# Optimization experiments

Measured on AMD Instinct MI355X. Metric: run time of the kernel, lower is better.

## Reference

```python
import jax, jax.numpy as jnp
import numpy as np

E = 768
H_HEADS = 12


def trilinear_border_sample(feat_map, coords):
    """grid_sample 3D, mode='bilinear', padding_mode='border', align_corners=True.
    feat_map: (B, C, D, H, W); coords: (B, P, 3) in [-1,1], last dim = (x, y, z) -> (W, H, D).
    Returns (B, P, C).
    """
    B, C, D, H, W = feat_map.shape
    x, y, z = coords[..., 0], coords[..., 1], coords[..., 2]
    ix = (x + 1.0) * 0.5 * (W - 1)
    iy = (y + 1.0) * 0.5 * (H - 1)
    iz = (z + 1.0) * 0.5 * (D - 1)
    x0 = jnp.floor(ix); y0 = jnp.floor(iy); z0 = jnp.floor(iz)
    wx = ix - x0; wy = iy - y0; wz = iz - z0
    x0i = jnp.clip(x0, 0, W - 1).astype(jnp.int32)
    x1i = jnp.clip(x0 + 1, 0, W - 1).astype(jnp.int32)
    y0i = jnp.clip(y0, 0, H - 1).astype(jnp.int32)
    y1i = jnp.clip(y0 + 1, 0, H - 1).astype(jnp.int32)
    z0i = jnp.clip(z0, 0, D - 1).astype(jnp.int32)
    z1i = jnp.clip(z0 + 1, 0, D - 1).astype(jnp.int32)
    flat = feat_map.reshape(B, C, D * H * W)

    def gather(zi, yi, xi):
        idx = (zi * H + yi) * W + xi  # (B, P)
        return jnp.take_along_axis(flat, idx[:, None, :], axis=2)  # (B, C, P)

    out = (
        gather(z0i, y0i, x0i) * ((1 - wz) * (1 - wy) * (1 - wx))[:, None, :]
        + gather(z0i, y0i, x1i) * ((1 - wz) * (1 - wy) * wx)[:, None, :]
        + gather(z0i, y1i, x0i) * ((1 - wz) * wy * (1 - wx))[:, None, :]
        + gather(z0i, y1i, x1i) * ((1 - wz) * wy * wx)[:, None, :]
        + gather(z1i, y0i, x0i) * (wz * (1 - wy) * (1 - wx))[:, None, :]
        + gather(z1i, y0i, x1i) * (wz * (1 - wy) * wx)[:, None, :]
        + gather(z1i, y1i, x0i) * (wz * wy * (1 - wx))[:, None, :]
        + gather(z1i, y1i, x1i) * (wz * wy * wx)[:, None, :]
    )
    return out.transpose(0, 2, 1)  # (B, P, C)


def setup_inputs() -> dict:
    key = jax.random.key(0)
    ks = jax.random.split(key, 12)
    B, fullN, nb = 64, 513, 32
    s = 1.0 / np.sqrt(E)
    return {
        "x": jax.random.normal(ks[0], (B, fullN, E), jnp.float32),
        "bio_embed": jax.random.normal(ks[1], (B, E), jnp.float32),
        "base_coords": jax.random.uniform(ks[2], (nb, 3), jnp.float32),
        "offsets": jax.random.normal(ks[3], (B, nb, 3), jnp.float32) * 0.1,
        "confidence": jax.random.uniform(ks[4], (B, 1), jnp.float32),
        "sample_proj_w": jax.random.uniform(ks[5], (E, E), jnp.float32, -s, s),
        "sample_proj_b": jax.random.uniform(ks[6], (E,), jnp.float32, -s, s),
        "in_proj_w": jax.random.uniform(ks[7], (3 * E, E), jnp.float32, -s, s),
        "in_proj_b": jnp.zeros((3 * E,), jnp.float32),
        "out_proj_w": jax.random.uniform(ks[8], (E, E), jnp.float32, -s, s),
        "out_proj_b": jnp.zeros((E,), jnp.float32),
        "grid_size": 8,
    }


def reference(x, bio_embed, base_coords, offsets, confidence,
              sample_proj_w, sample_proj_b, in_proj_w, in_proj_b,
              out_proj_w, out_proj_b, grid_size):
    B, fullN, C = x.shape
    G = grid_size
    patch_tokens = x[:, 1:, :]  # (B, N, C), N = G^3
    feat_map = patch_tokens.transpose(0, 2, 1).reshape(B, C, G, G, G)

    coords = jnp.clip(base_coords[None, :, :] + offsets, -1.0, 1.0)  # (B, nb, 3)
    sampled = trilinear_border_sample(feat_map, coords)  # (B, nb, C)
    sampled = sampled @ sample_proj_w.T + sample_proj_b

    # MultiheadAttention: single query (bio_embed), keys/values = sampled tokens
    hd = E // H_HEADS
    Wq, Wk, Wv = in_proj_w[:E], in_proj_w[E:2 * E], in_proj_w[2 * E:]
    bq, bk, bv = in_proj_b[:E], in_proj_b[E:2 * E], in_proj_b[2 * E:]
    q = (bio_embed @ Wq.T + bq).reshape(B, H_HEADS, hd)
    k = (sampled @ Wk.T + bk).reshape(B, -1, H_HEADS, hd)
    v = (sampled @ Wv.T + bv).reshape(B, -1, H_HEADS, hd)
    scores = jnp.einsum('bhd,bphd->bhp', q, k) / jnp.sqrt(jnp.asarray(hd, q.dtype))
    attn = jax.nn.softmax(scores, axis=-1)
    ctx = jnp.einsum('bhp,bphd->bhd', attn, v).reshape(B, E)
    attn_out = ctx @ out_proj_w.T + out_proj_b  # (B, E)

    out = jnp.broadcast_to(attn_out[:, None, :], (B, fullN, C))
    out = out * confidence[:, :, None]
    return out
```

## Files before the change

kernel.cpp:

```cpp
#include <hip/hip_runtime.h>
#include <hip/hip_bf16.h>
#include <math.h>

#define E 768
#define NH 12
#define HD 64

typedef __attribute__((ext_vector_type(8))) short bf16x8;
typedef __attribute__((ext_vector_type(4))) float f32x4;

__device__ __forceinline__ unsigned short f2bf_rne(float f) {
    unsigned int u = __float_as_uint(f);
    u += 0x7FFF + ((u >> 16) & 1);
    return (unsigned short)(u >> 16);
}

__global__ __launch_bounds__(256) void fused_conv_sample(
    const float* __restrict__ spw, const float* __restrict__ ipw,
    const float* __restrict__ x,
    const float* __restrict__ bcrd, const float* __restrict__ offs,
    const int* __restrict__ gsize,
    unsigned short* __restrict__ spw_bf, unsigned short* __restrict__ kvw_bf,
    unsigned short* __restrict__ sampled,
    int B, int P, int fullN, int nb_conv1, int nb_conv2)
{
    int blk = blockIdx.x;
    int t = threadIdx.x;

    if (blk < nb_conv1) {
        int i = blk * 256 + t;
        float4 v = ((const float4*)spw)[i];
        ushort4 o;
        o.x = f2bf_rne(v.x); o.y = f2bf_rne(v.y);
        o.z = f2bf_rne(v.z); o.w = f2bf_rne(v.w);
        ((ushort4*)spw_bf)[i] = o;
        return;
    }
    blk -= nb_conv1;
    if (blk < nb_conv2) {
        int i = blk * 256 + t;
        float4 v = ((const float4*)(ipw + (size_t)E * E))[i];
        ushort4 o;
        o.x = f2bf_rne(v.x); o.y = f2bf_rne(v.y);
        o.z = f2bf_rne(v.z); o.w = f2bf_rne(v.w);
        ((ushort4*)kvw_bf)[i] = o;
        return;
    }
    blk -= nb_conv2;
    {
        int bp = blk;
        int b = bp / P, p = bp % P;
        int G = *gsize;
        float gm1 = (float)(G - 1);

        float cx = bcrd[p * 3 + 0] + offs[bp * 3 + 0];
        float cy = bcrd[p * 3 + 1] + offs[bp * 3 + 1];
        float cz = bcrd[p * 3 + 2] + offs[bp * 3 + 2];
        cx = fminf(fmaxf(cx, -1.f), 1.f);
        cy = fminf(fmaxf(cy, -1.f), 1.f);
        cz = fminf(fmaxf(cz, -1.f), 1.f);

        float ix = (cx + 1.f) * 0.5f * gm1;
        float iy = (cy + 1.f) * 0.5f * gm1;
        float iz = (cz + 1.f) * 0.5f * gm1;
        float fx = floorf(ix), fy = floorf(iy), fz = floorf(iz);
        float wx = ix - fx, wy = iy - fy, wz = iz - fz;

        int x0 = (int)fminf(fmaxf(fx,       0.f), gm1);
        int x1 = (int)fminf(fmaxf(fx + 1.f, 0.f), gm1);
        int y0 = (int)fminf(fmaxf(fy,       0.f), gm1);
        int y1 = (int)fminf(fmaxf(fy + 1.f, 0.f), gm1);
        int z0 = (int)fminf(fmaxf(fz,       0.f), gm1);
        int z1 = (int)fminf(fmaxf(fz + 1.f, 0.f), gm1);

        int tk[8];
        tk[0] = (z0 * G + y0) * G + x0;
        tk[1] = (z0 * G + y0) * G + x1;
        tk[2] = (z0 * G + y1) * G + x0;
        tk[3] = (z0 * G + y1) * G + x1;
        tk[4] = (z1 * G + y0) * G + x0;
        tk[5] = (z1 * G + y0) * G + x1;
        tk[6] = (z1 * G + y1) * G + x0;
        tk[7] = (z1 * G + y1) * G + x1;
        float wgt[8];
        wgt[0] = (1.f - wz) * (1.f - wy) * (1.f - wx);
        wgt[1] = (1.f - wz) * (1.f - wy) * wx;
        wgt[2] = (1.f - wz) * wy * (1.f - wx);
        wgt[3] = (1.f - wz) * wy * wx;
        wgt[4] = wz * (1.f - wy) * (1.f - wx);
        wgt[5] = wz * (1.f - wy) * wx;
        wgt[6] = wz * wy * (1.f - wx);
        wgt[7] = wz * wy * wx;

        const float4* xb4 = (const float4*)(x + ((size_t)b * fullN + 1) * E);
        ushort4* outp = (ushort4*)(sampled + (size_t)bp * E);
        for (int c4 = t; c4 < E / 4; c4 += 256) {
            float4 acc = {0.f, 0.f, 0.f, 0.f};
#pragma unroll
            for (int k = 0; k < 8; ++k) {
                float4 v = xb4[(size_t)tk[k] * (E / 4) + c4];
                acc.x += wgt[k] * v.x; acc.y += wgt[k] * v.y;
                acc.z += wgt[k] * v.z; acc.w += wgt[k] * v.w;
            }
            ushort4 o;
            o.x = f2bf_rne(acc.x); o.y = f2bf_rne(acc.y);
            o.z = f2bf_rne(acc.z); o.w = f2bf_rne(acc.w);
            outp[c4] = o;
        }
    }
}

template <bool OUT_BF16>
__global__ __launch_bounds__(256) void gemm_bf16_nt(
    const unsigned short* __restrict__ A,
    const unsigned short* __restrict__ W,
    const float* __restrict__ bias,
    void* __restrict__ C,
    int M, int N, int K)
{
    __shared__ unsigned short lsA[128 * 32];
    __shared__ unsigned short lsB[128 * 32];

    int wv = threadIdx.x >> 6;
    int ln = threadIdx.x & 63;
    int m0 = blockIdx.y * 128;
    int n0 = blockIdx.x * 128;
    int wm = (wv & 1) * 64;
    int wn = (wv >> 1) * 64;

    f32x4 acc[4][4] = {};

    int srow = ln >> 2;
    int scol = (ln & 3) * 8;

    for (int k0 = 0; k0 < K; k0 += 32) {
#pragma unroll
        for (int c = 0; c < 2; ++c) {
            int chunk = wv * 2 + c;
            int row = chunk * 16 + srow;
            const unsigned short* ga = A + (size_t)(m0 + row) * K + k0 + scol;
            const unsigned short* gw = W + (size_t)(n0 + row) * K + k0 + scol;
            __builtin_amdgcn_global_load_lds(
                (const __attribute__((address_space(1))) unsigned int*)ga,
                (__attribute__((address_space(3))) unsigned int*)(lsA + chunk * 16 * 32),
                16, 0, 0);
            __builtin_amdgcn_global_load_lds(
                (const __attribute__((address_space(1))) unsigned int*)gw,
                (__attribute__((address_space(3))) unsigned int*)(lsB + chunk * 16 * 32),
                16, 0, 0);
        }
        __syncthreads();

        int kq = (ln >> 4) * 8;
        int rsel = ln & 15;
        bf16x8 af[4], bfr[4];
#pragma unroll
        for (int i = 0; i < 4; ++i) {
            af[i]  = *(const bf16x8*)&lsA[(wm + i * 16 + rsel) * 32 + kq];
            bfr[i] = *(const bf16x8*)&lsB[(wn + i * 16 + rsel) * 32 + kq];
        }
#pragma unroll
        for (int i = 0; i < 4; ++i)
#pragma unroll
            for (int j = 0; j < 4; ++j)
                acc[i][j] = __builtin_amdgcn_mfma_f32_16x16x32_bf16(
                    af[i], bfr[j], acc[i][j], 0, 0, 0);
        __syncthreads();
    }

    int cr = (ln >> 4) * 4;
    int cc = ln & 15;
#pragma unroll
    for (int j = 0; j < 4; ++j) {
        int col = n0 + wn + j * 16 + cc;
        float bv = bias[col];
#pragma unroll
        for (int i = 0; i < 4; ++i) {
#pragma unroll
            for (int r = 0; r < 4; ++r) {
                int row = m0 + wm + i * 16 + cr + r;
                float v = acc[i][j][r] + bv;
                if (OUT_BF16)
                    ((unsigned short*)C)[(size_t)row * N + col] = f2bf_rne(v);
                else
                    ((float*)C)[(size_t)row * N + col] = v;
            }
        }
    }
}

__global__ void matvec_nt(const float* __restrict__ A,
                          const float* __restrict__ W,
                          const float* __restrict__ bias,
                          float* __restrict__ C,
                          int M, int N, int K)
{
    int wid = blockIdx.x * (blockDim.x >> 6) + (threadIdx.x >> 6);
    int ln = threadIdx.x & 63;
    if (wid >= M * N) return;
    int m = wid / N, n = wid % N;
    const float* a = A + (size_t)m * K;
    const float* w = W + (size_t)n * K;
    float s = 0.f;
    for (int k = ln; k < K; k += 64) s += a[k] * w[k];
#pragma unroll
    for (int off = 32; off; off >>= 1) s += __shfl_down(s, off);
    if (ln == 0) C[wid] = s + bias[n];
}

__global__ void attn_kernel(const float* __restrict__ q,
                            const float* __restrict__ kv,
                            float* __restrict__ ctx,
                            int B, int P)
{
    int bh = blockIdx.x;
    int b = bh / NH, h = bh % NH;
    int d = threadIdx.x;

    __shared__ float qs[HD];
    __shared__ float sc[64];

    qs[d] = q[(size_t)b * E + h * HD + d];
    __syncthreads();

    if (d < P) {
        const float* kr = kv + ((size_t)(b * P + d)) * (2 * E) + h * HD;
        float s = 0.f;
#pragma unroll
        for (int e = 0; e < HD; ++e) s += qs[e] * kr[e];
        sc[d] = s * 0.125f;
    }
    __syncthreads();

    float mx = -INFINITY;
    for (int p = 0; p < P; ++p) mx = fmaxf(mx, sc[p]);
    float den = 0.f;
    for (int p = 0; p < P; ++p) den += __expf(sc[p] - mx);
    __syncthreads();
    if (d < P) sc[d] = __expf(sc[d] - mx) / den;
    __syncthreads();

    float acc = 0.f;
    for (int p = 0; p < P; ++p)
        acc += sc[p] * kv[((size_t)(b * P + p)) * (2 * E) + E + h * HD + d];
    ctx[(size_t)b * E + h * HD + d] = acc;
}

__global__ void bcast_kernel(const float* __restrict__ attn_out,
                             const float* __restrict__ conf,
                             float* __restrict__ out,
                             int fullN, int pc)
{
    int b = blockIdx.y;
    float cf = conf[b];
    const float4* ao = (const float4*)(attn_out + (size_t)b * E);
    float4* ob = (float4*)(out + (size_t)b * fullN * E);
    int i = blockIdx.x * blockDim.x + threadIdx.x;
    if (i < pc) {
        int c4 = i % (E / 4);
        float4 v = ao[c4];
        v.x *= cf; v.y *= cf; v.z *= cf; v.w *= cf;
        ob[i] = v;
    }
}

extern "C" void kernel_launch(void* const* d_in, const int* in_sizes, int n_in,
                              void* d_out, int out_size, void* d_ws, size_t ws_size,
                              hipStream_t stream)
{
    const float* x      = (const float*)d_in[0];
    const float* bio    = (const float*)d_in[1];
    const float* bcrd   = (const float*)d_in[2];
    const float* offs   = (const float*)d_in[3];
    const float* conf   = (const float*)d_in[4];
    const float* spw    = (const float*)d_in[5];
    const float* spb    = (const float*)d_in[6];
    const float* ipw    = (const float*)d_in[7];
    const float* ipb    = (const float*)d_in[8];
    const float* opw    = (const float*)d_in[9];
    const float* opb    = (const float*)d_in[10];
    const int*   gsize  = (const int*)d_in[11];
    float* out = (float*)d_out;

    const int B     = in_sizes[1] / E;
    const int P     = in_sizes[2] / 3;
    const int fullN = in_sizes[0] / (B * E);
    const int M     = B * P;

    char* base = (char*)d_out;
    unsigned short* sampled_bf = (unsigned short*)(base + 0);
    unsigned short* sproj_bf   = (unsigned short*)(base + 3145728);
    unsigned short* spw_bf     = (unsigned short*)(base + 6291456);
    unsigned short* ipwkv_bf   = (unsigned short*)(base + 7471104);
    float*          kv         = (float*)(base + 9830400);
    float*          q          = (float*)(base + 22413312);
    float*          ctx        = (float*)(base + 22609920);
    float*          aout       = (float*)d_ws;

    int nb_conv1 = (E * E) / 1024;
    int nb_conv2 = (2 * E * E) / 1024;
    int nblocks  = nb_conv1 + nb_conv2 + M;
    fused_conv_sample<<<nblocks, 256, 0, stream>>>(spw, ipw, x, bcrd, offs, gsize,
                                                   spw_bf, ipwkv_bf, sampled_bf,
                                                   B, P, fullN, nb_conv1, nb_conv2);

    gemm_bf16_nt<true><<<dim3(E / 128, M / 128), 256, 0, stream>>>(
        sampled_bf, spw_bf, spb, sproj_bf, M, E, E);

    gemm_bf16_nt<false><<<dim3(2 * E / 128, M / 128), 256, 0, stream>>>(
        sproj_bf, ipwkv_bf, ipb + E, kv, M, 2 * E, E);

    {
        int tot = B * E;
        matvec_nt<<<(tot + 3) / 4, 256, 0, stream>>>(bio, ipw, ipb, q, B, E, E);
    }

    attn_kernel<<<B * NH, 64, 0, stream>>>(q, kv, ctx, B, P);

    {
        int tot = B * E;
        matvec_nt<<<(tot + 3) / 4, 256, 0, stream>>>(ctx, opw, opb, aout, B, E, E);
    }

    int pc = fullN * E / 4;
    bcast_kernel<<<dim3((pc + 255) / 256, B), 256, 0, stream>>>(aout, conf, out, fullN, pc);
}
```

Baseline: 305.6 us.

## Fuse q-projection into prep kernel and out-projection into attention via atomics

The query projection matvec and zeroing of the attention output buffer move into the first prep kernel as extra block ranges. The separate out-projection matvec is removed: each (batch, head) attention block multiplies its 64-dim context slice by the matching out-proj weight columns and atomically adds partial sums into the output. The out-proj bias is added in the broadcast kernel. This cuts two launches and the ctx round trip, at the cost of 12-way float atomics per output element and non-deterministic summation order.

```diff
diff --git a/kernel.cpp b/kernel.cpp
--- a/kernel.cpp
+++ b/kernel.cpp
@@ -15,14 +15,15 @@
     return (unsigned short)(u >> 16);
 }
 
-__global__ __launch_bounds__(256) void fused_conv_sample(
+__global__ __launch_bounds__(256) void fused_pre(
     const float* __restrict__ spw, const float* __restrict__ ipw,
-    const float* __restrict__ x,
+    const float* __restrict__ ipb, const float* __restrict__ x,
     const float* __restrict__ bcrd, const float* __restrict__ offs,
-    const int* __restrict__ gsize,
+    const int* __restrict__ gsize, const float* __restrict__ bio,
     unsigned short* __restrict__ spw_bf, unsigned short* __restrict__ kvw_bf,
-    unsigned short* __restrict__ sampled,
-    int B, int P, int fullN, int nb_conv1, int nb_conv2)
+    unsigned short* __restrict__ sampled, float* __restrict__ q,
+    float* __restrict__ aout,
+    int B, int P, int fullN, int nb_conv1, int nb_conv2, int nb_qproj)
 {
     int blk = blockIdx.x;
     int t = threadIdx.x;
@@ -47,7 +48,7 @@
         return;
     }
     blk -= nb_conv2;
-    {
+    if (blk < B * P) {
         int bp = blk;
         int b = bp / P, p = bp % P;
         int G = *gsize;
@@ -107,6 +108,27 @@
             o.z = f2bf_rne(acc.z); o.w = f2bf_rne(acc.w);
             outp[c4] = o;
         }
+        return;
+    }
+    blk -= B * P;
+    if (blk < nb_qproj) {
+        int wid = blk * 4 + (t >> 6);
+        int ln = t & 63;
+        int m = wid / E, n = wid % E;
+        const float* a = bio + (size_t)m * E;
+        const float* w = ipw + (size_t)n * E;
+        float s = 0.f;
+        for (int k = ln; k < E; k += 64) s += a[k] * w[k];
+#pragma unroll
+        for (int off = 32; off; off >>= 1) s += __shfl_down(s, off);
+        if (ln == 0) q[wid] = s + ipb[n];
+        return;
+    }
+    blk -= nb_qproj;
+    {
+        int i = blk * 256 + t;
+        float4 z = {0.f, 0.f, 0.f, 0.f};
+        ((float4*)aout)[i] = z;
     }
 }
 
@@ -189,29 +211,11 @@
     }
 }
 
-__global__ void matvec_nt(const float* __restrict__ A,
-                          const float* __restrict__ W,
-                          const float* __restrict__ bias,
-                          float* __restrict__ C,
-                          int M, int N, int K)
-{
-    int wid = blockIdx.x * (blockDim.x >> 6) + (threadIdx.x >> 6);
-    int ln = threadIdx.x & 63;
-    if (wid >= M * N) return;
-    int m = wid / N, n = wid % N;
-    const float* a = A + (size_t)m * K;
-    const float* w = W + (size_t)n * K;
-    float s = 0.f;
-    for (int k = ln; k < K; k += 64) s += a[k] * w[k];
-#pragma unroll
-    for (int off = 32; off; off >>= 1) s += __shfl_down(s, off);
-    if (ln == 0) C[wid] = s + bias[n];
-}
-
-__global__ void attn_kernel(const float* __restrict__ q,
-                            const float* __restrict__ kv,
-                            float* __restrict__ ctx,
-                            int B, int P)
+__global__ void attn_op_kernel(const float* __restrict__ q,
+                               const float* __restrict__ kv,
+                               const float* __restrict__ opw,
+                               float* __restrict__ aout,
+                               int B, int P)
 {
     int bh = blockIdx.x;
     int b = bh / NH, h = bh % NH;
@@ -219,6 +223,7 @@
 
     __shared__ float qs[HD];
     __shared__ float sc[64];
+    __shared__ float cv[HD];
 
     qs[d] = q[(size_t)b * E + h * HD + d];
     __syncthreads();
@@ -243,23 +248,43 @@
     float acc = 0.f;
     for (int p = 0; p < P; ++p)
         acc += sc[p] * kv[((size_t)(b * P + p)) * (2 * E) + E + h * HD + d];
-    ctx[(size_t)b * E + h * HD + d] = acc;
-}
-
-__global__ void bcast_kernel(const float* __restrict__ attn_out,
+    cv[d] = acc;
+    __syncthreads();
+
+    float* ab = aout + (size_t)b * E;
+#pragma unroll
+    for (int nn = 0; nn < E / 64; ++nn) {
+        int n = nn * 64 + d;
+        const float4* w4 = (const float4*)(opw + (size_t)n * E + h * HD);
+        float s = 0.f;
+#pragma unroll
+        for (int k4 = 0; k4 < HD / 4; ++k4) {
+            float4 w = w4[k4];
+            s += w.x * cv[k4 * 4] + w.y * cv[k4 * 4 + 1]
+               + w.z * cv[k4 * 4 + 2] + w.w * cv[k4 * 4 + 3];
+        }
+        atomicAdd(&ab[n], s);
+    }
+}
+
+__global__ void bcast_kernel(const float* __restrict__ aout,
+                             const float* __restrict__ opb,
                              const float* __restrict__ conf,
                              float* __restrict__ out,
                              int fullN, int pc)
 {
     int b = blockIdx.y;
     float cf = conf[b];
-    const float4* ao = (const float4*)(attn_out + (size_t)b * E);
+    const float4* ao = (const float4*)(aout + (size_t)b * E);
+    const float4* bo = (const float4*)opb;
     float4* ob = (float4*)(out + (size_t)b * fullN * E);
     int i = blockIdx.x * blockDim.x + threadIdx.x;
     if (i < pc) {
         int c4 = i % (E / 4);
         float4 v = ao[c4];
-        v.x *= cf; v.y *= cf; v.z *= cf; v.w *= cf;
+        float4 bb = bo[c4];
+        v.x = (v.x + bb.x) * cf; v.y = (v.y + bb.y) * cf;
+        v.z = (v.z + bb.z) * cf; v.w = (v.w + bb.w) * cf;
         ob[i] = v;
     }
 }
@@ -294,15 +319,16 @@
     unsigned short* ipwkv_bf   = (unsigned short*)(base + 7471104);
     float*          kv         = (float*)(base + 9830400);
     float*          q          = (float*)(base + 22413312);
-    float*          ctx        = (float*)(base + 22609920);
     float*          aout       = (float*)d_ws;
 
     int nb_conv1 = (E * E) / 1024;
     int nb_conv2 = (2 * E * E) / 1024;
-    int nblocks  = nb_conv1 + nb_conv2 + M;
-    fused_conv_sample<<<nblocks, 256, 0, stream>>>(spw, ipw, x, bcrd, offs, gsize,
-                                                   spw_bf, ipwkv_bf, sampled_bf,
-                                                   B, P, fullN, nb_conv1, nb_conv2);
+    int nb_qproj = (B * E) / 4;
+    int nb_zero  = (B * E) / 1024;
+    int nblocks  = nb_conv1 + nb_conv2 + M + nb_qproj + nb_zero;
+    fused_pre<<<nblocks, 256, 0, stream>>>(spw, ipw, ipb, x, bcrd, offs, gsize, bio,
+                                           spw_bf, ipwkv_bf, sampled_bf, q, aout,
+                                           B, P, fullN, nb_conv1, nb_conv2, nb_qproj);
 
     gemm_bf16_nt<true><<<dim3(E / 128, M / 128), 256, 0, stream>>>(
         sampled_bf, spw_bf, spb, sproj_bf, M, E, E);
@@ -310,18 +336,9 @@
     gemm_bf16_nt<false><<<dim3(2 * E / 128, M / 128), 256, 0, stream>>>(
         sproj_bf, ipwkv_bf, ipb + E, kv, M, 2 * E, E);
 
-    {
-        int tot = B * E;
-        matvec_nt<<<(tot + 3) / 4, 256, 0, stream>>>(bio, ipw, ipb, q, B, E, E);
-    }
-
-    attn_kernel<<<B * NH, 64, 0, stream>>>(q, kv, ctx, B, P);
-
-    {
-        int tot = B * E;
-        matvec_nt<<<(tot + 3) / 4, 256, 0, stream>>>(ctx, opw, opb, aout, B, E, E);
-    }
+    attn_op_kernel<<<B * NH, 64, 0, stream>>>(q, kv, opw, aout, B, P);
 
     int pc = fullN * E / 4;
-    bcast_kernel<<<dim3((pc + 255) / 256, B), 256, 0, stream>>>(aout, conf, out, fullN, pc);
-}
+    bcast_kernel<<<dim3((pc + 255) / 256, B), 256, 0, stream>>>(aout, opb, conf,
+                                                                out, fullN, pc);
+}
```

After: 316.3 us. 3.5% more time.
